# Kernel optimization log

Hardware: AMD Instinct MI355X
Metric: run time of the kernel (lower is better)

The kernel has to match this reference:

```python
import jax, jax.numpy as jnp
import numpy as np

H = 16      # attention_head_num
DH = 64     # attention_head_size
D = H * DH  # out_dim = 1024


def setup_inputs() -> dict:
    key = jax.random.key(0)
    ks = jax.random.split(key, 9)
    s = 1.0 / np.sqrt(D)
    x = jax.random.normal(ks[0], (2, 2048, D), dtype=jnp.float32)
    Wq = jax.random.uniform(ks[1], (D, D), jnp.float32, -s, s)
    bq = jax.random.uniform(ks[2], (D,), jnp.float32, -s, s)
    Wk = jax.random.uniform(ks[3], (D, D), jnp.float32, -s, s)
    bk = jax.random.uniform(ks[4], (D,), jnp.float32, -s, s)
    Wv = jax.random.uniform(ks[5], (D, D), jnp.float32, -s, s)
    bv = jax.random.uniform(ks[6], (D,), jnp.float32, -s, s)
    Wo = jax.random.uniform(ks[7], (D, D), jnp.float32, -s, s)
    bo = jax.random.uniform(ks[8], (D,), jnp.float32, -s, s)
    return {"x": x, "Wq": Wq, "bq": bq, "Wk": Wk, "bk": bk,
            "Wv": Wv, "bv": bv, "Wo": Wo, "bo": bo}


def reference(x, Wq, bq, Wk, bk, Wv, bv, Wo, bo):
    B, S, _ = x.shape
    # projections (nn.Linear: x @ W^T + b)
    q = (x @ Wq.T + bq).reshape(B, S, H, DH).transpose(0, 2, 1, 3)  # [B,H,S,Dh]
    k = (x @ Wk.T + bk).reshape(B, S, H, DH).transpose(0, 2, 1, 3)
    v = (x @ Wv.T + bv).reshape(B, S, H, DH).transpose(0, 2, 1, 3)
    scores = jnp.einsum('bhqd,bhkd->bhqk', q, k) / jnp.sqrt(jnp.float32(DH))
    probs = jax.nn.softmax(scores, axis=-1)  # dropout is identity in eval mode
    ctx = jnp.einsum('bhqk,bhkd->bhqd', probs, v)
    ctx = ctx.transpose(0, 2, 1, 3).reshape(B, S, D)
    return ctx @ Wo.T + bo
```

## Files before the change

kernel.cpp:

```cpp
#include <hip/hip_runtime.h>
#include <hip/hip_bf16.h>
#include <stdint.h>

typedef __attribute__((ext_vector_type(8))) short bf16x8;
typedef __attribute__((ext_vector_type(8))) unsigned short u16x8;
typedef __attribute__((ext_vector_type(4))) unsigned short u16x4;
typedef __attribute__((ext_vector_type(4))) float f32x4;

constexpr int NB  = 2;
constexpr int NS  = 2048;
constexpr int NH  = 16;
constexpr int NDH = 64;
constexpr int ND  = 1024;

static __device__ __forceinline__ unsigned short bfbits(float f) {
    union { float f; uint32_t u; } v; v.f = f;
    uint32_t u = v.u + 0x7FFFu + ((v.u >> 16) & 1u);
    return (unsigned short)(u >> 16);
}

static __device__ __forceinline__ float fexp2(float x) {
#if __has_builtin(__builtin_amdgcn_exp2f)
    return __builtin_amdgcn_exp2f(x);
#else
    return exp2f(x);
#endif
}

static __device__ __forceinline__ void gl_lds16(const void* g, void* l) {
    __builtin_amdgcn_global_load_lds(
        (const __attribute__((address_space(1))) unsigned int*)g,
        (__attribute__((address_space(3))) unsigned int*)l, 16, 0, 0);
}

__global__ __launch_bounds__(256)
void cvt_kernel(const float* __restrict__ x,  const float* __restrict__ wq,
                const float* __restrict__ wk, const float* __restrict__ wv,
                const float* __restrict__ wo,
                unsigned short* __restrict__ xb,  unsigned short* __restrict__ wqb,
                unsigned short* __restrict__ wkb, unsigned short* __restrict__ wvb,
                unsigned short* __restrict__ wob)
{
    const int b = blockIdx.x;
    const float* s; unsigned short* d; int off;
    if      (b < 2048) { s = x;  d = xb;  off = b; }
    else if (b < 2560) { s = wq; d = wqb; off = b - 2048; }
    else if (b < 3072) { s = wk; d = wkb; off = b - 2560; }
    else if (b < 3584) { s = wv; d = wvb; off = b - 3072; }
    else               { s = wo; d = wob; off = b - 3584; }
    const size_t idx = ((size_t)off * 256 + threadIdx.x) * 8;
    float4 f0 = *(const float4*)&s[idx];
    float4 f1 = *(const float4*)&s[idx + 4];
    u16x8 o;
    o[0] = bfbits(f0.x); o[1] = bfbits(f0.y); o[2] = bfbits(f0.z); o[3] = bfbits(f0.w);
    o[4] = bfbits(f1.x); o[5] = bfbits(f1.y); o[6] = bfbits(f1.z); o[7] = bfbits(f1.w);
    *(u16x8*)&d[idx] = o;
}

__global__ __launch_bounds__(256, 2)
void qkv_kernel(const unsigned short* __restrict__ xb,
                const unsigned short* __restrict__ wqb,
                const unsigned short* __restrict__ wkb,
                const unsigned short* __restrict__ wvb,
                const float* __restrict__ bq, const float* __restrict__ bk,
                const float* __restrict__ bv,
                unsigned short* __restrict__ qbuf,
                unsigned short* __restrict__ kbuf,
                unsigned short* __restrict__ vtbuf)
{
    __shared__ unsigned short As[128 * 64];
    __shared__ unsigned short Bs[128 * 64];
    __shared__ unsigned short Tt[128][136];

    const int fid = blockIdx.x + blockIdx.y * 24;
    const int xcd = fid & 7, idx = fid >> 3;
    const int bx  = idx >> 2;
    const int by  = xcd * 4 + (idx & 3);

    const int m0  = by * 128;
    const int jg0 = bx * 128;
    const int proj = jg0 >> 10;
    const int n0   = jg0 & 1023;
    const unsigned short* W = (proj == 0) ? wqb : (proj == 1) ? wkb : wvb;
    const float* bias       = (proj == 0) ? bq  : (proj == 1) ? bk  : bv;

    const int tid = threadIdx.x, lane = tid & 63, wid = tid >> 6;
    const int wm = wid >> 1, wn = wid & 1;
    const int l15 = lane & 15, g = lane >> 4;

    const f32x4 fzero = {0.f, 0.f, 0.f, 0.f};
    f32x4 acc[4][4];
#pragma unroll
    for (int i = 0; i < 4; i++)
#pragma unroll
        for (int j = 0; j < 4; j++) acc[i][j] = fzero;

    const int srow = tid >> 3;
    const int scb  = ((tid & 7) * 16) ^ ((srow & 7) << 4);
    const char* asrc = (const char*)xb + (size_t)(m0 + srow) * 2048 + scb;
    const char* bsrc = (const char*)W  + (size_t)(n0 + srow) * 2048 + scb;
    char* adst = (char*)As + tid * 16;
    char* bdst = (char*)Bs + tid * 16;
    const int xm = (l15 & 7) << 4;

    for (int k0 = 0; k0 < 1024; k0 += 64) {
#pragma unroll
        for (int i = 0; i < 4; i++) {
            gl_lds16(asrc + (size_t)i * 32 * 2048 + k0 * 2, adst + i * 4096);
            gl_lds16(bsrc + (size_t)i * 32 * 2048 + k0 * 2, bdst + i * 4096);
        }
        __syncthreads();
#pragma unroll
        for (int kk = 0; kk < 2; kk++) {
            bf16x8 af[4], bfr[4];
#pragma unroll
            for (int i = 0; i < 4; i++) {
                const int row = wm * 64 + i * 16 + l15;
                af[i] = *(const bf16x8*)((const char*)As + row * 128 + ((kk * 64 + g * 16) ^ xm));
            }
#pragma unroll
            for (int j = 0; j < 4; j++) {
                const int row = wn * 64 + j * 16 + l15;
                bfr[j] = *(const bf16x8*)((const char*)Bs + row * 128 + ((kk * 64 + g * 16) ^ xm));
            }
#pragma unroll
            for (int i = 0; i < 4; i++)
#pragma unroll
                for (int j = 0; j < 4; j++)
                    acc[i][j] = __builtin_amdgcn_mfma_f32_16x16x32_bf16(af[i], bfr[j], acc[i][j], 0, 0, 0);
        }
        __syncthreads();
    }

    if (proj < 2) {
        unsigned short* qk_out = (proj == 0) ? qbuf : kbuf;
        const float qs = (proj == 0) ? 0.18033688f : 1.0f;
#pragma unroll
        for (int j = 0; j < 4; j++) {
            const int col = n0 + wn * 64 + j * 16 + l15;
            const float bsv = bias[col];
            const int h = col >> 6, dh = col & 63;
#pragma unroll
            for (int i = 0; i < 4; i++)
#pragma unroll
                for (int r = 0; r < 4; r++) {
                    const int row = m0 + wm * 64 + i * 16 + g * 4 + r;
                    const int b_ = row >> 11, s_ = row & (NS - 1);
                    qk_out[((size_t)((b_ * NH + h) * NS + s_)) * NDH + dh] =
                        bfbits((acc[i][j][r] + bsv) * qs);
                }
        }
    } else {
#pragma unroll
        for (int j = 0; j < 4; j++) {
            const int cl = wn * 64 + j * 16 + l15;
            const float bsv = bias[n0 + cl];
#pragma unroll
            for (int i = 0; i < 4; i++) {
                u16x4 w4;
#pragma unroll
                for (int r = 0; r < 4; r++) w4[r] = bfbits(acc[i][j][r] + bsv);
                *(u16x4*)&Tt[cl][wm * 64 + i * 16 + g * 4] = w4;
            }
        }
        __syncthreads();
        const int b_ = m0 >> 11, s0 = m0 & (NS - 1);
        const int h0 = n0 >> 6;
#pragma unroll
        for (int it = 0; it < 8; it++) {
            const int c = wid * 32 + it * 4 + g;
            u16x8 v8 = *(const u16x8*)&Tt[c][l15 * 8];
            const size_t row = (size_t)(b_ * NH + h0 + (c >> 6)) * NDH + (c & 63);
            *(u16x8*)&vtbuf[row * NS + s0 + l15 * 8] = v8;
        }
    }
}

__global__ __launch_bounds__(256, 4)
void attn_kernel(const unsigned short* __restrict__ qbuf,
                 const unsigned short* __restrict__ kbuf,
                 const unsigned short* __restrict__ vtbuf,
                 unsigned short* __restrict__ ctxbuf)
{
    __shared__ char smem[32768];
    char* kbase = smem;
    char* vbase = smem + 16384;

    const int fid  = blockIdx.x + blockIdx.y * 32;
    const int nid  = (fid & 7) * 128 + (fid >> 3);
    const int bx   = nid & 31, bh = nid >> 5;
    const int q0   = bx * 64;

    const int tid = threadIdx.x, lane = tid & 63, wid = tid >> 6;
    const int l15 = lane & 15, g = lane >> 4;
    const int qh = wid >> 1, ks = wid & 1;

    const unsigned short* qb = qbuf  + (size_t)bh * NS * NDH;
    const unsigned short* kb = kbuf  + (size_t)bh * NS * NDH;
    const unsigned short* vb = vtbuf + (size_t)bh * NDH * NS;

    bf16x8 qf[2][2];
#pragma unroll
    for (int qg = 0; qg < 2; qg++) {
        const int qrow = q0 + qh * 32 + qg * 16 + l15;
        qf[qg][0] = *(const bf16x8*)&qb[(size_t)qrow * NDH + g * 8];
        qf[qg][1] = *(const bf16x8*)&qb[(size_t)qrow * NDH + 32 + g * 8];
    }

    const short oneb = (short)0x3F80;
    const bf16x8 ones = {oneb, oneb, oneb, oneb, oneb, oneb, oneb, oneb};

    const f32x4 fzero = {0.f, 0.f, 0.f, 0.f};
    f32x4 acc[2][4];
#pragma unroll
    for (int qg = 0; qg < 2; qg++)
#pragma unroll
        for (int d = 0; d < 4; d++) acc[qg][d] = fzero;
    f32x4 acc_l[2] = {fzero, fzero};

    const int o = tid * 16;
    const int srow = o >> 7;
    const int scb  = (o & 127) ^ ((srow & 7) << 4);
    const char* ksrc  = (const char*)kb + srow * 128 + scb;
    const char* ksrc2 = (const char*)kb + (srow + 32) * 128 + scb;
    const char* vsrc  = (const char*)vb + (size_t)srow * (NS * 2) + scb;
    const char* vsrc2 = (const char*)vb + (size_t)(srow + 32) * (NS * 2) + scb;
    const int xm = (l15 & 7) << 4;

    auto STAGE = [&](int b, int t_) {
        gl_lds16(ksrc  + (size_t)t_ * 8192, kbase + b * 8192 + o);
        gl_lds16(ksrc2 + (size_t)t_ * 8192, kbase + b * 8192 + 4096 + o);
        gl_lds16(vsrc  + (size_t)t_ * 128,  vbase + b * 8192 + o);
        gl_lds16(vsrc2 + (size_t)t_ * 128,  vbase + b * 8192 + 4096 + o);
    };

    STAGE(0, 0);
    asm volatile("s_waitcnt vmcnt(0)" ::: "memory");
    __builtin_amdgcn_s_barrier();
    asm volatile("" ::: "memory");

    for (int t = 0; t < 32; t++) {
        const int cb = t & 1;
        if (t < 31) STAGE(cb ^ 1, t + 1);

        const char* ksb = kbase + cb * 8192;
        const char* vsb = vbase + cb * 8192;

        f32x4 sv[2][2];
#pragma unroll
        for (int kt = 0; kt < 2; kt++) {
            const int row = ks * 32 + kt * 16 + l15;
            const char* rb = ksb + row * 128;
            bf16x8 kf0 = *(const bf16x8*)(rb + ((g * 16) ^ xm));
            bf16x8 kf1 = *(const bf16x8*)(rb + ((64 + g * 16) ^ xm));
#pragma unroll
            for (int qg = 0; qg < 2; qg++) {
                f32x4 s4 = fzero;
                s4 = __builtin_amdgcn_mfma_f32_16x16x32_bf16(kf0, qf[qg][0], s4, 0, 0, 0);
                s4 = __builtin_amdgcn_mfma_f32_16x16x32_bf16(kf1, qf[qg][1], s4, 0, 0, 0);
                sv[qg][kt] = s4;
            }
        }

#pragma unroll
        for (int qg = 0; qg < 2; qg++)
#pragma unroll
            for (int kt = 0; kt < 2; kt++)
#pragma unroll
                for (int r = 0; r < 4; r++)
                    sv[qg][kt][r] = fexp2(sv[qg][kt][r]);

        bf16x8 pf[2];
#pragma unroll
        for (int qg = 0; qg < 2; qg++) {
            union { __hip_bfloat162 h2; uint32_t u; } c0, c1, c2, c3;
            float2 p01 = { sv[qg][0][0], sv[qg][0][1] };
            float2 p23 = { sv[qg][0][2], sv[qg][0][3] };
            float2 p45 = { sv[qg][1][0], sv[qg][1][1] };
            float2 p67 = { sv[qg][1][2], sv[qg][1][3] };
            c0.h2 = __float22bfloat162_rn(p01);
            c1.h2 = __float22bfloat162_rn(p23);
            c2.h2 = __float22bfloat162_rn(p45);
            c3.h2 = __float22bfloat162_rn(p67);
            uint32_t a0 = c0.u, a1 = c1.u, b0 = c2.u, b1 = c3.u;
            asm("v_permlane32_swap_b32 %0, %1" : "+v"(a0), "+v"(b0));
            asm("v_permlane32_swap_b32 %0, %1" : "+v"(a1), "+v"(b1));
            asm("v_permlane16_swap_b32 %0, %1" : "+v"(a0), "+v"(b0));
            asm("v_permlane16_swap_b32 %0, %1" : "+v"(a1), "+v"(b1));
            union { uint32_t w[4]; bf16x8 fr; } r_;
            r_.w[0] = a0; r_.w[1] = a1; r_.w[2] = b0; r_.w[3] = b1;
            pf[qg] = r_.fr;
        }

#pragma unroll
        for (int qg = 0; qg < 2; qg++)
            acc_l[qg] = __builtin_amdgcn_mfma_f32_16x16x32_bf16(pf[qg], ones, acc_l[qg], 0, 0, 0);
#pragma unroll
        for (int d = 0; d < 4; d++) {
            const int row = d * 16 + l15;
            const char* rb = vsb + row * 128;
            bf16x8 vf = *(const bf16x8*)(rb + ((ks * 64 + g * 16) ^ xm));
#pragma unroll
            for (int qg = 0; qg < 2; qg++)
                acc[qg][d] = __builtin_amdgcn_mfma_f32_16x16x32_bf16(pf[qg], vf, acc[qg][d], 0, 0, 0);
        }

        asm volatile("s_waitcnt vmcnt(0)" ::: "memory");
        __builtin_amdgcn_s_barrier();
        asm volatile("" ::: "memory");
    }

    if (ks == 1) {
#pragma unroll
        for (int qg = 0; qg < 2; qg++)
#pragma unroll
            for (int d = 0; d < 4; d++)
                *(f32x4*)(smem + qh * 10240 + ((qg * 4 + d) * 64 + lane) * 16) = acc[qg][d];
#pragma unroll
        for (int qg = 0; qg < 2; qg++)
            *(f32x4*)(smem + qh * 10240 + 8192 + (qg * 64 + lane) * 16) = acc_l[qg];
    }
    __syncthreads();
    if (ks == 0) {
#pragma unroll
        for (int qg = 0; qg < 2; qg++) {
#pragma unroll
            for (int d = 0; d < 4; d++)
                acc[qg][d] += *(const f32x4*)(smem + qh * 10240 + ((qg * 4 + d) * 64 + lane) * 16);
            acc_l[qg] += *(const f32x4*)(smem + qh * 10240 + 8192 + (qg * 64 + lane) * 16);
        }

        const int b_ = bh >> 4, h_ = bh & 15;
#pragma unroll
        for (int qg = 0; qg < 2; qg++)
#pragma unroll
            for (int r = 0; r < 4; r++) {
                const float inv = 1.f / acc_l[qg][r];
                const int sq = q0 + qh * 32 + qg * 16 + g * 4 + r;
                const size_t base = ((size_t)(b_ * NS + sq)) * ND + h_ * NDH;
#pragma unroll
                for (int d = 0; d < 4; d++)
                    ctxbuf[base + d * 16 + l15] = bfbits(acc[qg][d][r] * inv);
            }
    }
}

__global__ __launch_bounds__(256, 2)
void out_kernel(const unsigned short* __restrict__ ctx,
                const unsigned short* __restrict__ wob,
                const float* __restrict__ bo,
                float* __restrict__ out)
{
    __shared__ unsigned short As[128 * 64];
    __shared__ unsigned short Bs[128 * 64];

    const int n0 = blockIdx.x * 128;
    const int m0 = blockIdx.y * 128;
    const int tid = threadIdx.x, lane = tid & 63, wid = tid >> 6;
    const int wm = wid >> 1, wn = wid & 1;
    const int l15 = lane & 15, g = lane >> 4;

    const f32x4 fzero = {0.f, 0.f, 0.f, 0.f};
    f32x4 acc[4][4];
#pragma unroll
    for (int i = 0; i < 4; i++)
#pragma unroll
        for (int j = 0; j < 4; j++) acc[i][j] = fzero;

    const int srow = tid >> 3;
    const int scb  = ((tid & 7) * 16) ^ ((srow & 7) << 4);
    const char* asrc = (const char*)ctx + (size_t)(m0 + srow) * 2048 + scb;
    const char* bsrc = (const char*)wob + (size_t)(n0 + srow) * 2048 + scb;
    char* adst = (char*)As + tid * 16;
    char* bdst = (char*)Bs + tid * 16;
    const int xm = (l15 & 7) << 4;

    for (int k0 = 0; k0 < 1024; k0 += 64) {
#pragma unroll
        for (int i = 0; i < 4; i++) {
            gl_lds16(asrc + (size_t)i * 32 * 2048 + k0 * 2, adst + i * 4096);
            gl_lds16(bsrc + (size_t)i * 32 * 2048 + k0 * 2, bdst + i * 4096);
        }
        __syncthreads();
#pragma unroll
        for (int kk = 0; kk < 2; kk++) {
            bf16x8 af[4], bfr[4];
#pragma unroll
            for (int i = 0; i < 4; i++) {
                const int row = wm * 64 + i * 16 + l15;
                af[i] = *(const bf16x8*)((const char*)As + row * 128 + ((kk * 64 + g * 16) ^ xm));
            }
#pragma unroll
            for (int j = 0; j < 4; j++) {
                const int row = wn * 64 + j * 16 + l15;
                bfr[j] = *(const bf16x8*)((const char*)Bs + row * 128 + ((kk * 64 + g * 16) ^ xm));
            }
#pragma unroll
            for (int i = 0; i < 4; i++)
#pragma unroll
                for (int j = 0; j < 4; j++)
                    acc[i][j] = __builtin_amdgcn_mfma_f32_16x16x32_bf16(af[i], bfr[j], acc[i][j], 0, 0, 0);
        }
        __syncthreads();
    }

#pragma unroll
    for (int j = 0; j < 4; j++) {
        const int col = n0 + wn * 64 + j * 16 + l15;
        const float bsv = bo[col];
#pragma unroll
        for (int i = 0; i < 4; i++)
#pragma unroll
            for (int r = 0; r < 4; r++) {
                const int row = m0 + wm * 64 + i * 16 + g * 4 + r;
                out[(size_t)row * ND + col] = acc[i][j][r] + bsv;
            }
    }
}

extern "C" void kernel_launch(void* const* d_in, const int* in_sizes, int n_in,
                              void* d_out, int out_size, void* d_ws, size_t ws_size,
                              hipStream_t stream) {
    const float* x  = (const float*)d_in[0];
    const float* Wq = (const float*)d_in[1];
    const float* bq = (const float*)d_in[2];
    const float* Wk = (const float*)d_in[3];
    const float* bk = (const float*)d_in[4];
    const float* Wv = (const float*)d_in[5];
    const float* bv = (const float*)d_in[6];
    const float* Wo = (const float*)d_in[7];
    const float* bo = (const float*)d_in[8];
    float* out = (float*)d_out;

    const size_t qk_elems = (size_t)NB * NH * NS * NDH;
    const size_t w_elems  = (size_t)ND * ND;
    unsigned short* qbuf   = (unsigned short*)d_ws;
    unsigned short* kbuf   = qbuf + qk_elems;
    unsigned short* vtbuf  = kbuf + qk_elems;
    unsigned short* ctxbuf = vtbuf + qk_elems;
    unsigned short* xb     = ctxbuf + qk_elems;
    unsigned short* wqb    = xb + qk_elems;
    unsigned short* wkb    = wqb + w_elems;
    unsigned short* wvb    = wkb + w_elems;
    unsigned short* wob    = wvb + w_elems;

    cvt_kernel<<<4096, 256, 0, stream>>>(x, Wq, Wk, Wv, Wo, xb, wqb, wkb, wvb, wob);
    qkv_kernel<<<dim3(24, 32), 256, 0, stream>>>(xb, wqb, wkb, wvb, bq, bk, bv,
                                                 qbuf, kbuf, vtbuf);
    attn_kernel<<<dim3(32, 32), 256, 0, stream>>>(qbuf, kbuf, vtbuf, ctxbuf);
    out_kernel<<<dim3(8, 32), 256, 0, stream>>>(ctxbuf, wob, bo, out);
}
```

Measured before the change: 114.0 us.

## Alias QKV shared memory and stage Q/K epilogue through LDS for vector stores

Aliases the transpose buffer onto the A/B tile shared memory to cut the LDS footprint, and raises the launch-bounds occupancy hint from 2 to 3 blocks. The Q/K epilogue now writes results into the shared tile first and then emits 16-byte coalesced row stores instead of scattered 2-byte global stores. The trade-offs are an extra barrier and LDS round trip, plus tighter register limits that could cause spills.

New measurement: 107.6 us. 1.06x faster.

```diff
diff --git a/kernel.cpp b/kernel.cpp
--- a/kernel.cpp
+++ b/kernel.cpp
@@ -57,7 +57,7 @@
     *(u16x8*)&d[idx] = o;
 }
 
-__global__ __launch_bounds__(256, 2)
+__global__ __launch_bounds__(256, 3)
 void qkv_kernel(const unsigned short* __restrict__ xb,
                 const unsigned short* __restrict__ wqb,
                 const unsigned short* __restrict__ wkb,
@@ -68,9 +68,10 @@
                 unsigned short* __restrict__ kbuf,
                 unsigned short* __restrict__ vtbuf)
 {
-    __shared__ unsigned short As[128 * 64];
-    __shared__ unsigned short Bs[128 * 64];
-    __shared__ unsigned short Tt[128][136];
+    __shared__ char smem[34816];
+    char* As = smem;
+    char* Bs = smem + 16384;
+    unsigned short (*Tt)[136] = (unsigned short(*)[136])smem;
 
     const int fid = blockIdx.x + blockIdx.y * 24;
     const int xcd = fid & 7, idx = fid >> 3;
@@ -99,8 +100,8 @@
     const int scb  = ((tid & 7) * 16) ^ ((srow & 7) << 4);
     const char* asrc = (const char*)xb + (size_t)(m0 + srow) * 2048 + scb;
     const char* bsrc = (const char*)W  + (size_t)(n0 + srow) * 2048 + scb;
-    char* adst = (char*)As + tid * 16;
-    char* bdst = (char*)Bs + tid * 16;
+    char* adst = As + tid * 16;
+    char* bdst = Bs + tid * 16;
     const int xm = (l15 & 7) << 4;
 
     for (int k0 = 0; k0 < 1024; k0 += 64) {
@@ -116,12 +117,12 @@
 #pragma unroll
             for (int i = 0; i < 4; i++) {
                 const int row = wm * 64 + i * 16 + l15;
-                af[i] = *(const bf16x8*)((const char*)As + row * 128 + ((kk * 64 + g * 16) ^ xm));
+                af[i] = *(const bf16x8*)(As + row * 128 + ((kk * 64 + g * 16) ^ xm));
             }
 #pragma unroll
             for (int j = 0; j < 4; j++) {
                 const int row = wn * 64 + j * 16 + l15;
-                bfr[j] = *(const bf16x8*)((const char*)Bs + row * 128 + ((kk * 64 + g * 16) ^ xm));
+                bfr[j] = *(const bf16x8*)(Bs + row * 128 + ((kk * 64 + g * 16) ^ xm));
             }
 #pragma unroll
             for (int i = 0; i < 4; i++)
@@ -137,18 +138,24 @@
         const float qs = (proj == 0) ? 0.18033688f : 1.0f;
 #pragma unroll
         for (int j = 0; j < 4; j++) {
-            const int col = n0 + wn * 64 + j * 16 + l15;
-            const float bsv = bias[col];
-            const int h = col >> 6, dh = col & 63;
+            const int col = wn * 64 + j * 16 + l15;
+            const float bsv = bias[n0 + col];
 #pragma unroll
             for (int i = 0; i < 4; i++)
 #pragma unroll
-                for (int r = 0; r < 4; r++) {
-                    const int row = m0 + wm * 64 + i * 16 + g * 4 + r;
-                    const int b_ = row >> 11, s_ = row & (NS - 1);
-                    qk_out[((size_t)((b_ * NH + h) * NS + s_)) * NDH + dh] =
+                for (int r = 0; r < 4; r++)
+                    Tt[wm * 64 + i * 16 + g * 4 + r][col] =
                         bfbits((acc[i][j][r] + bsv) * qs);
-                }
+        }
+        __syncthreads();
+        const int b_ = m0 >> 11, s0 = m0 & (NS - 1);
+        const int h0 = n0 >> 6;
+        const int h  = h0 + (l15 >> 3), dh0 = (l15 * 8) & 63;
+#pragma unroll
+        for (int it = 0; it < 8; it++) {
+            const int row = wid * 32 + it * 4 + g;
+            u16x8 v8 = *(const u16x8*)&Tt[row][l15 * 8];
+            *(u16x8*)&qk_out[((size_t)((b_ * NH + h) * NS + s0 + row)) * NDH + dh0] = v8;
         }
     } else {
 #pragma unroll
```
